# Kernel optimization log

Hardware: AMD Instinct MI355X
Metric: run time of the kernel (lower is better)

## Reference

```python
import jax, jax.numpy as jnp
import numpy as np

B, C, T = 4, 256, 4096
EPS = 1e-5
NEG = -1e8


def setup_inputs() -> dict:
    key = jax.random.key(0)
    ks = jax.random.split(key, 12)
    s = 1.0 / np.sqrt(C)
    x = jax.random.normal(ks[0], (B, C, T), dtype=jnp.float32)
    x_mask = (jax.random.uniform(ks[1], (B, 1, T)) > 0.1).astype(jnp.float32)
    return {
        "x": x,
        "x_mask": x_mask,
        # Normalize params
        "gamma": jnp.ones((C,), jnp.float32),
        "beta": jnp.zeros((C,), jnp.float32),
        "Wp": jax.random.normal(ks[2], (C, C), jnp.float32) * s,
        "bp": jnp.zeros((C,), jnp.float32),
        # 1x1 conv projections (weight [C_out, C_in])
        "Wq": jax.random.normal(ks[3], (C, C), jnp.float32) * s,
        "bq": jnp.zeros((C,), jnp.float32),
        "Wk": jax.random.normal(ks[4], (C, C), jnp.float32) * s,
        "bk": jnp.zeros((C,), jnp.float32),
        "Wv": jax.random.normal(ks[5], (C, C), jnp.float32) * s,
        "bv": jnp.zeros((C,), jnp.float32),
        "Wo": jax.random.normal(ks[6], (C, C), jnp.float32) * s,
        "bo": jnp.zeros((C,), jnp.float32),
    }


def _conv1x1(W, b, x):
    # x: [B, C, T] -> [B, C, T]
    return jnp.einsum('oc,bct->bot', W, x) + b[None, :, None]


def reference(x, x_mask, gamma, beta, Wp, bp, Wq, bq, Wk, bk, Wv, bv, Wo, bo):
    m = x_mask  # [B,1,T]
    h = x * m
    # Normalize: layer_norm over channel dim + linear, operating on [B,T,C]
    ht = h.transpose(0, 2, 1)  # [B,T,C]
    mu = jnp.mean(ht, axis=-1, keepdims=True)
    var = jnp.mean(jnp.square(ht - mu), axis=-1, keepdims=True)
    ln = (ht - mu) * jax.lax.rsqrt(var + EPS) * gamma + beta
    ln = ln @ Wp.T + bp
    h = ln.transpose(0, 2, 1) * m  # [B,C,T]

    q = _conv1x1(Wq, bq, h) * m
    k = _conv1x1(Wk, bk, h) * m
    v = _conv1x1(Wv, bv, h) * m

    scale = float(C) ** (-0.5)
    # scores[b,t,s] = sum_c q[b,c,t] k[b,c,s]
    w = jnp.einsum('bct,bcs->bts', q, k) * scale
    neg = (1.0 - m) * NEG  # [B,1,T]
    w = w + neg + neg.transpose(0, 2, 1)  # mask keys and queries
    w = jax.nn.softmax(w, axis=2)
    # h_[b,c,t] = sum_s v[b,c,s] w[b,t,s]
    h = jnp.einsum('bcs,bts->bct', v, w)
    h = _conv1x1(Wo, bo, h) * m
    return (x + h) * m
```

## Files before the change

kernel.cpp:

```cpp
#include <hip/hip_runtime.h>

#define Bn 4
#define Cn 256
#define Tn 4096

typedef unsigned short u16;
typedef __bf16 bf16x8 __attribute__((ext_vector_type(8)));
typedef float f32x4 __attribute__((ext_vector_type(4)));
typedef float f32x16 __attribute__((ext_vector_type(16)));
typedef u16 u16x8 __attribute__((ext_vector_type(8)));

__device__ __forceinline__ float b2f(u16 u) {
    union { unsigned int i; float f; } v;
    v.i = ((unsigned int)u) << 16;
    return v.f;
}
__device__ __forceinline__ u16 f2b(float f) {
    union { float f; unsigned int i; } v;
    v.f = f;
    unsigned int r = v.i + 0x7FFFu + ((v.i >> 16) & 1u);
    return (u16)(r >> 16);
}
__device__ __forceinline__ bf16x8 ones8() {
    union { u16 u[8]; bf16x8 v; } t;
    for (int j = 0; j < 8; j++) t.u[j] = 0x3F80;
    return t.v;
}

__global__ __launch_bounds__(256) void cvt_kernel(
    const float* __restrict__ w0, const float* __restrict__ w1,
    const float* __restrict__ w2, const float* __restrict__ w3,
    const float* __restrict__ w4, u16* __restrict__ dst)
{
    int gid = blockIdx.x * 256 + threadIdx.x;
    int base = gid * 4;
    int region = base >> 16;
    int off = base & 65535;
    const float* src = region == 0 ? w0 : region == 1 ? w1
                     : region == 2 ? w2 : region == 3 ? w3 : w4;
    float sc = (region == 1) ? 0.0625f : 1.0f;
    float4 v = *(const float4*)(src + off);
    ushort4 o;
    o.x = f2b(v.x * sc); o.y = f2b(v.y * sc);
    o.z = f2b(v.z * sc); o.w = f2b(v.w * sc);
    *(ushort4*)(dst + base) = o;
}

__global__ __launch_bounds__(256) void ln_kernel(
    const float* __restrict__ x, const float* __restrict__ mask,
    const float* __restrict__ gamma, const float* __restrict__ beta,
    u16* __restrict__ lnT, u16* __restrict__ xb)
{
    __shared__ __attribute__((aligned(16))) u16 tile[32][264];
    __shared__ float ssum[8][32], ssq[8][32], smu[32], srs[32];
    const int tid = threadIdx.x;
    const int b = blockIdx.y;
    const int t0 = blockIdx.x * 32;
    const int g = tid >> 5, tl = tid & 31;
    const int t = t0 + tl;
    const float mval = mask[b * Tn + t];
    float s = 0.f, s2 = 0.f;
    for (int c = g; c < Cn; c += 8) {
        float v = x[((size_t)(b * Cn + c)) * Tn + t] * mval;
        s += v; s2 += v * v;
        u16 vb = f2b(v);
        tile[tl][c] = vb;
        xb[((size_t)(b * Cn + c)) * Tn + t] = vb;
    }
    ssum[g][tl] = s; ssq[g][tl] = s2;
    __syncthreads();
    if (tid < 32) {
        float su = 0.f, sq = 0.f;
        for (int k = 0; k < 8; k++) { su += ssum[k][tid]; sq += ssq[k][tid]; }
        float mu = su * (1.f / Cn);
        float var = sq * (1.f / Cn) - mu * mu;
        var = fmaxf(var, 0.0f);
        smu[tid] = mu;
        srs[tid] = 1.0f / sqrtf(var + 1e-5f);
    }
    __syncthreads();
    for (int it = 0; it < 4; it++) {
        int idx = it * 256 + tid;
        int row = idx >> 5, c16 = idx & 31;
        float mu = smu[row], rs = srs[row];
        u16x8 ov;
        for (int j = 0; j < 8; j++) {
            int c = c16 * 8 + j;
            float h = b2f(tile[row][c]);
            float v = (h - mu) * rs * gamma[c] + beta[c];
            ov[j] = f2b(v);
        }
        *(u16x8*)(lnT + ((size_t)(b * Tn + t0 + row)) * Cn + c16 * 8) = ov;
    }
}

__global__ __launch_bounds__(256) void wp_kernel(
    const u16* __restrict__ Xb, const u16* __restrict__ Wb,
    const float* __restrict__ bias, const float* __restrict__ mask,
    u16* __restrict__ Yout)
{
    __shared__ __attribute__((aligned(16))) u16 Al[128][72];
    __shared__ __attribute__((aligned(16))) u16 Bl[64][72];
    const int tid = threadIdx.x;
    const int b = blockIdx.z;
    const int m0 = blockIdx.x * 128;
    const int n0 = blockIdx.y * 64;
    const int wave = tid >> 6, lane = tid & 63;
    const int ln16 = lane & 15, quad = lane >> 4;
    const int wm = (wave & 1) * 64, wn = (wave >> 1) * 32;

    const u16* Abase = Xb + ((size_t)(b * Tn + m0)) * Cn;
    const u16* Bbase = Wb + (size_t)n0 * Cn;

    f32x4 acc[4][2];
    for (int i = 0; i < 4; i++)
        for (int j = 0; j < 2; j++) acc[i][j] = (f32x4){0.f, 0.f, 0.f, 0.f};

    for (int k0 = 0; k0 < Cn; k0 += 64) {
        for (int it = 0; it < 4; it++) {
            int idx = it * 256 + tid;
            int row = idx >> 3, gg = idx & 7;
            *(uint4*)(&Al[row][gg * 8]) =
                *(const uint4*)(Abase + (size_t)row * Cn + k0 + gg * 8);
        }
        for (int it = 0; it < 2; it++) {
            int idx = it * 256 + tid;
            int row = idx >> 3, gg = idx & 7;
            *(uint4*)(&Bl[row][gg * 8]) =
                *(const uint4*)(Bbase + (size_t)row * Cn + k0 + gg * 8);
        }
        __syncthreads();
        for (int kk = 0; kk < 2; kk++) {
            bf16x8 af[4], bfr[2];
            for (int i = 0; i < 4; i++)
                af[i] = *(const bf16x8*)(&Al[wm + i * 16 + ln16][kk * 32 + quad * 8]);
            for (int j = 0; j < 2; j++)
                bfr[j] = *(const bf16x8*)(&Bl[wn + j * 16 + ln16][kk * 32 + quad * 8]);
            for (int i = 0; i < 4; i++)
                for (int j = 0; j < 2; j++)
                    acc[i][j] = __builtin_amdgcn_mfma_f32_16x16x32_bf16(
                        af[i], bfr[j], acc[i][j], 0, 0, 0);
        }
        __syncthreads();
    }
    for (int i = 0; i < 4; i++) {
        for (int j = 0; j < 2; j++) {
            int nn = n0 + wn + j * 16 + ln16;
            for (int r = 0; r < 4; r++) {
                int tt = m0 + wm + i * 16 + quad * 4 + r;
                float val = acc[i][j][r] + bias[nn];
                val *= mask[b * Tn + tt];
                Yout[((size_t)(b * Tn + tt)) * Cn + nn] = f2b(val);
            }
        }
    }
}

__global__ __launch_bounds__(256) void qkv_kernel(
    const u16* __restrict__ h1T,
    const u16* __restrict__ Wq_, const float* __restrict__ bq_,
    const u16* __restrict__ Wk_, const float* __restrict__ bk_,
    const u16* __restrict__ Wv_, const float* __restrict__ bv_,
    const float* __restrict__ mask,
    u16* __restrict__ qO, u16* __restrict__ kO, u16* __restrict__ vO)
{
    __shared__ __attribute__((aligned(16))) u16 Al[128][72];
    __shared__ __attribute__((aligned(16))) u16 Bl[64][72];
    const int tid = threadIdx.x;
    const int z = blockIdx.z;
    const int which = z >> 2;
    const int b = z & 3;
    const u16* W = which == 0 ? Wq_ : which == 1 ? Wk_ : Wv_;
    const float* bi = which == 0 ? bq_ : which == 1 ? bk_ : bv_;
    const float bsc = which == 0 ? 0.0625f : 1.0f;
    const int m0 = blockIdx.x * 128;
    const int n0 = blockIdx.y * 64;
    const int wave = tid >> 6, lane = tid & 63;
    const int ln16 = lane & 15, quad = lane >> 4;
    const int wm = (wave & 1) * 64, wn = (wave >> 1) * 32;

    const u16* Abase = h1T + ((size_t)(b * Tn + m0)) * Cn;
    const u16* Bbase = W + (size_t)n0 * Cn;

    f32x4 acc[4][2];
    for (int i = 0; i < 4; i++)
        for (int j = 0; j < 2; j++) acc[i][j] = (f32x4){0.f, 0.f, 0.f, 0.f};

    for (int k0 = 0; k0 < Cn; k0 += 64) {
        for (int it = 0; it < 4; it++) {
            int idx = it * 256 + tid;
            int row = idx >> 3, gg = idx & 7;
            *(uint4*)(&Al[row][gg * 8]) =
                *(const uint4*)(Abase + (size_t)row * Cn + k0 + gg * 8);
        }
        for (int it = 0; it < 2; it++) {
            int idx = it * 256 + tid;
            int row = idx >> 3, gg = idx & 7;
            *(uint4*)(&Bl[row][gg * 8]) =
                *(const uint4*)(Bbase + (size_t)row * Cn + k0 + gg * 8);
        }
        __syncthreads();
        for (int kk = 0; kk < 2; kk++) {
            bf16x8 af[4], bfr[2];
            for (int i = 0; i < 4; i++)
                af[i] = *(const bf16x8*)(&Al[wm + i * 16 + ln16][kk * 32 + quad * 8]);
            for (int j = 0; j < 2; j++)
                bfr[j] = *(const bf16x8*)(&Bl[wn + j * 16 + ln16][kk * 32 + quad * 8]);
            for (int i = 0; i < 4; i++)
                for (int j = 0; j < 2; j++)
                    acc[i][j] = __builtin_amdgcn_mfma_f32_16x16x32_bf16(
                        af[i], bfr[j], acc[i][j], 0, 0, 0);
        }
        __syncthreads();
    }

    if (which < 2) {
        u16* Yo = which == 0 ? qO : kO;
        for (int i = 0; i < 4; i++) {
            for (int j = 0; j < 2; j++) {
                int nn = n0 + wn + j * 16 + ln16;
                for (int r = 0; r < 4; r++) {
                    int tt = m0 + wm + i * 16 + quad * 4 + r;
                    float val = acc[i][j][r] + bi[nn] * bsc;
                    val *= mask[b * Tn + tt];
                    Yo[((size_t)(b * Tn + tt)) * Cn + nn] = f2b(val);
                }
            }
        }
    } else {
        u16* vt = &Al[0][0];
        for (int i = 0; i < 4; i++) {
            for (int j = 0; j < 2; j++) {
                int nl = wn + j * 16 + ln16;
                for (int r = 0; r < 4; r++) {
                    int ml = wm + i * 16 + quad * 4 + r;
                    int tt = m0 + ml;
                    float val = acc[i][j][r] + bi[n0 + nl];
                    val *= mask[b * Tn + tt];
                    vt[nl * 136 + ml] = f2b(val);
                }
            }
        }
        __syncthreads();
        for (int itc = 0; itc < 4; itc++) {
            int cidx = itc * 256 + tid;
            int row = cidx >> 4;
            int ch = cidx & 15;
            u16x8 ov = *(const u16x8*)(vt + row * 136 + ch * 8);
            *(u16x8*)(vO + ((size_t)(b * Cn + n0 + row)) * Tn + m0 + ch * 8) = ov;
        }
    }
}

__global__ __launch_bounds__(512, 2) void attn_kernel(
    const u16* __restrict__ qT, const u16* __restrict__ kT,
    const u16* __restrict__ vv, const float* __restrict__ mask,
    u16* __restrict__ PO01, u16* __restrict__ POx, float* __restrict__ pL)
{
    __shared__ __attribute__((aligned(16))) u16 kls[2][32][264];
    __shared__ __attribute__((aligned(16))) u16 vls[2][256][40];
    __shared__ __attribute__((aligned(16))) u16 pls[8][32][40];
    __shared__ float nls[1024];
    const int tid = threadIdx.x;
    const int id = blockIdx.x;
    const int spl = id & 3;
    const int b = (id >> 2) & 3;
    const int qb = id >> 4;
    const int t0 = qb * 256;
    const int wave = tid >> 6, lane = tid & 63;
    const int ln32 = lane & 31, half = lane >> 5;
    const int sBeg = spl * (Tn / 4);
    const int nIter = (Tn / 4) / 32;

    for (int i = tid; i < 1024; i += 512)
        nls[i] = (1.0f - mask[b * Tn + sBeg + i]) * -1e8f - 8.0f;

    bf16x8 qf[16];
    {
        const u16* qp = qT + ((size_t)(b * Tn + t0 + wave * 32 + ln32)) * Cn + half * 8;
        for (int ks = 0; ks < 16; ks++) qf[ks] = *(const bf16x8*)(qp + ks * 16);
    }
    f32x16 acc[8], lac;
    for (int i = 0; i < 16; i++) lac[i] = 0.f;
    for (int nt = 0; nt < 8; nt++) acc[nt] = lac;
    const bf16x8 ones = ones8();

    uint4 kpre[2], vpre[2];
    auto loadK = [&](int s0) {
        for (int i = 0; i < 2; i++) {
            int idx = i * 512 + tid;
            kpre[i] = *(const uint4*)(kT + ((size_t)(b * Tn + s0 + (idx >> 5))) * Cn + (idx & 31) * 8);
        }
    };
    auto loadV = [&](int s0) {
        for (int i = 0; i < 2; i++) {
            int idx = i * 512 + tid;
            vpre[i] = *(const uint4*)(vv + ((size_t)(b * Cn + (idx >> 2))) * Tn + s0 + (idx & 3) * 8);
        }
    };
    loadK(sBeg);
    loadV(sBeg);

    for (int it = 0; it < nIter; it++) {
        const int s0 = sBeg + it * 32;
        const int cb = it & 1;
        for (int i = 0; i < 2; i++) {
            int idx = i * 512 + tid;
            *(uint4*)(&kls[cb][idx >> 5][(idx & 31) * 8]) = kpre[i];
        }
        for (int i = 0; i < 2; i++) {
            int idx = i * 512 + tid;
            *(uint4*)(&vls[cb][idx >> 2][(idx & 3) * 8]) = vpre[i];
        }
        if (it + 1 < nIter) {
            loadK(s0 + 32);
            loadV(s0 + 32);
        }
        __syncthreads();
        const float negk = nls[it * 32 + ln32];

        f32x16 S;
        for (int i = 0; i < 16; i++) S[i] = 0.f;
        for (int ks = 0; ks < 16; ks++) {
            bf16x8 kf = *(const bf16x8*)(&kls[cb][ln32][ks * 16 + half * 8]);
            S = __builtin_amdgcn_mfma_f32_32x32x16_bf16(qf[ks], kf, S, 0, 0, 0);
        }
        for (int r = 0; r < 16; r++) S[r] = __expf(S[r] + negk);
        for (int r = 0; r < 16; r++) {
            int row = (r & 3) + 8 * (r >> 2) + 4 * half;
            pls[wave][row][ln32] = f2b(S[r]);
        }
        bf16x8 pf0 = *(const bf16x8*)(&pls[wave][ln32][half * 8]);
        bf16x8 pf1 = *(const bf16x8*)(&pls[wave][ln32][16 + half * 8]);
        lac = __builtin_amdgcn_mfma_f32_32x32x16_bf16(pf0, ones, lac, 0, 0, 0);
        lac = __builtin_amdgcn_mfma_f32_32x32x16_bf16(pf1, ones, lac, 0, 0, 0);
        for (int nt = 0; nt < 8; nt++) {
            bf16x8 v0 = *(const bf16x8*)(&vls[cb][nt * 32 + ln32][half * 8]);
            bf16x8 v1 = *(const bf16x8*)(&vls[cb][nt * 32 + ln32][16 + half * 8]);
            acc[nt] = __builtin_amdgcn_mfma_f32_32x32x16_bf16(pf0, v0, acc[nt], 0, 0, 0);
            acc[nt] = __builtin_amdgcn_mfma_f32_32x32x16_bf16(pf1, v1, acc[nt], 0, 0, 0);
        }
    }
    const size_t SZe = (size_t)Bn * Tn * Cn;
    u16* myPO = (spl < 2) ? PO01 + (size_t)spl * SZe
                          : POx + (size_t)(spl - 2) * SZe;
    for (int r = 0; r < 16; r++) {
        int trow = (r & 3) + 8 * (r >> 2) + 4 * half;
        int t = t0 + wave * 32 + trow;
        for (int nt = 0; nt < 8; nt++)
            myPO[((size_t)(b * Tn + t)) * Cn + nt * 32 + ln32] = f2b(acc[nt][r]);
        if (ln32 == 0) pL[(size_t)spl * (Bn * Tn) + b * Tn + t] = lac[r];
    }
}

__global__ __launch_bounds__(256) void final_kernel(
    const u16* __restrict__ WoB, const float* __restrict__ bo,
    const u16* __restrict__ PO01, const u16* __restrict__ POx,
    const float* __restrict__ pL,
    const float* __restrict__ mask, const u16* __restrict__ xb,
    float* __restrict__ out)
{
    __shared__ __attribute__((aligned(16))) u16 Al[128][72];
    __shared__ __attribute__((aligned(16))) u16 Bl[64][72];
    __shared__ float rls[64];
    const int tid = threadIdx.x;
    const int b = blockIdx.z;
    const int m0 = blockIdx.x * 128;
    const int n0 = blockIdx.y * 64;
    const int wave = tid >> 6, lane = tid & 63;
    const int ln16 = lane & 15, quad = lane >> 4;
    const int wm = (wave & 1) * 64, wn = (wave >> 1) * 32;
    const size_t BT = (size_t)Bn * Tn;
    const size_t SZe = BT * Cn;

    if (tid < 64) {
        size_t R = (size_t)b * Tn + n0 + tid;
        float l = pL[R] + pL[BT + R] + pL[2 * BT + R] + pL[3 * BT + R];
        rls[tid] = 1.0f / fmaxf(l, 1e-30f);
    }

    f32x4 acc[4][2];
    for (int i = 0; i < 4; i++)
        for (int j = 0; j < 2; j++) acc[i][j] = (f32x4){0.f, 0.f, 0.f, 0.f};

    for (int k0 = 0; k0 < Cn; k0 += 64) {
        for (int it = 0; it < 4; it++) {
            int idx = it * 256 + tid;
            int row = idx >> 3, gg = idx & 7;
            *(uint4*)(&Al[row][gg * 8]) =
                *(const uint4*)(WoB + (size_t)(m0 + row) * Cn + k0 + gg * 8);
        }
        for (int it = 0; it < 2; it++) {
            int idx = it * 256 + tid;
            int row = idx >> 3, gg = idx & 7;
            size_t base = ((size_t)b * Tn + n0 + row) * Cn + k0 + gg * 8;
            u16x8 a0 = *(const u16x8*)(PO01 + base);
            u16x8 a1 = *(const u16x8*)(PO01 + SZe + base);
            u16x8 a2 = *(const u16x8*)(POx + base);
            u16x8 a3 = *(const u16x8*)(POx + SZe + base);
            u16x8 o;
            for (int j = 0; j < 8; j++)
                o[j] = f2b(b2f(a0[j]) + b2f(a1[j]) + b2f(a2[j]) + b2f(a3[j]));
            *(u16x8*)(&Bl[row][gg * 8]) = o;
        }
        __syncthreads();
        for (int kk = 0; kk < 2; kk++) {
            bf16x8 af[4], bfr[2];
            for (int i = 0; i < 4; i++)
                af[i] = *(const bf16x8*)(&Al[wm + i * 16 + ln16][kk * 32 + quad * 8]);
            for (int j = 0; j < 2; j++)
                bfr[j] = *(const bf16x8*)(&Bl[wn + j * 16 + ln16][kk * 32 + quad * 8]);
            for (int i = 0; i < 4; i++)
                for (int j = 0; j < 2; j++)
                    acc[i][j] = __builtin_amdgcn_mfma_f32_16x16x32_bf16(
                        af[i], bfr[j], acc[i][j], 0, 0, 0);
        }
        __syncthreads();
    }
    for (int i = 0; i < 4; i++) {
        for (int j = 0; j < 2; j++) {
            int nl = wn + j * 16 + ln16;
            int tt = n0 + nl;
            float rl = rls[nl];
            float mk = mask[b * Tn + tt];
            for (int r = 0; r < 4; r++) {
                int oo = m0 + wm + i * 16 + quad * 4 + r;
                float val = acc[i][j][r] * rl + bo[oo];
                float xr = b2f(xb[((size_t)(b * Cn + oo)) * Tn + tt]);
                out[((size_t)(b * Cn + oo)) * Tn + tt] = (xr + val) * mk;
            }
        }
    }
}

extern "C" void kernel_launch(void* const* d_in, const int* in_sizes, int n_in,
                              void* d_out, int out_size, void* d_ws, size_t ws_size,
                              hipStream_t stream)
{
    const float* x     = (const float*)d_in[0];
    const float* xmask = (const float*)d_in[1];
    const float* gamma = (const float*)d_in[2];
    const float* beta  = (const float*)d_in[3];
    const float* Wp = (const float*)d_in[4];
    const float* bp = (const float*)d_in[5];
    const float* Wq = (const float*)d_in[6];
    const float* bq = (const float*)d_in[7];
    const float* Wk = (const float*)d_in[8];
    const float* bk = (const float*)d_in[9];
    const float* Wv = (const float*)d_in[10];
    const float* bv = (const float*)d_in[11];
    const float* Wo = (const float*)d_in[12];
    const float* bo = (const float*)d_in[13];
    float* out = (float*)d_out;

    u16* ws = (u16*)d_ws;
    const size_t SZ = (size_t)Bn * Tn * Cn;
    const size_t WSZ = (size_t)Cn * Cn;
    const size_t BT = (size_t)Bn * Tn;
    u16* lnT = ws;
    u16* h1T = ws + SZ;
    u16* qTt = ws + 2 * SZ;
    u16* kTt = ws + 3 * SZ;
    u16* vB  = ws + 4 * SZ;
    u16* wbf = ws + 5 * SZ;
    u16* PO01 = ws;
    u16* POx  = ws + 5 * SZ + 5 * WSZ;
    float* pL = (float*)(POx + 2 * SZ);
    u16* xb   = (u16*)(pL + 4 * BT);

    u16* WpB = wbf;
    u16* WqB = wbf + WSZ;
    u16* WkB = wbf + 2 * WSZ;
    u16* WvB = wbf + 3 * WSZ;
    u16* WoB = wbf + 4 * WSZ;

    dim3 blk(256);
    cvt_kernel<<<dim3(320), blk, 0, stream>>>(Wp, Wq, Wk, Wv, Wo, wbf);
    ln_kernel<<<dim3(Tn / 32, Bn), blk, 0, stream>>>(x, xmask, gamma, beta, lnT, xb);
    wp_kernel<<<dim3(Tn / 128, Cn / 64, Bn), blk, 0, stream>>>(
        lnT, WpB, bp, xmask, h1T);
    qkv_kernel<<<dim3(Tn / 128, Cn / 64, 3 * Bn), blk, 0, stream>>>(
        h1T, WqB, bq, WkB, bk, WvB, bv, xmask, qTt, kTt, vB);
    attn_kernel<<<dim3(256), dim3(512), 0, stream>>>(
        qTt, kTt, vB, xmask, PO01, POx, pL);
    final_kernel<<<dim3(Cn / 128, Tn / 64, Bn), blk, 0, stream>>>(
        WoB, bo, PO01, POx, pL, xmask, xb, out);
}
```

Measured before the change: 245.6 us.

## Register-prefetch GEMM tiles, keep attention P in registers, relax barriers

The projection, QKV and output GEMMs now load the next K-tile from global memory into registers before the barrier, so the fetch overlaps the current MFMA work. __syncthreads is replaced by a barrier that waits only on LDS counters, so outstanding global prefetches are not drained. In the attention kernel, QK^T is computed transposed so the exp'd scores can be packed to bf16 with v_cvt_pk_bf16_f32 and rearranged with v_permlane32_swap, which removes the LDS round-trip and the pls buffer. s_setprio hints raise wave priority around MFMA blocks. The cost is more register pressure, and correctness now depends on the custom barrier and on the lane mapping of the permlane swap.

Result: slower. 315.8 us (+28.6%).

```diff
diff --git a/kernel.cpp b/kernel.cpp
--- a/kernel.cpp
+++ b/kernel.cpp
@@ -25,6 +25,21 @@
     union { u16 u[8]; bf16x8 v; } t;
     for (int j = 0; j < 8; j++) t.u[j] = 0x3F80;
     return t.v;
+}
+
+__device__ __forceinline__ void barrier_nodrain() {
+    asm volatile("s_waitcnt lgkmcnt(0)" ::: "memory");
+    __builtin_amdgcn_s_barrier();
+    asm volatile("" ::: "memory");
+}
+
+__device__ __forceinline__ unsigned int cvtpk(float lo, float hi) {
+    unsigned int r;
+    asm("v_cvt_pk_bf16_f32 %0, %1, %2" : "=v"(r) : "v"(lo), "v"(hi));
+    return r;
+}
+__device__ __forceinline__ void permswap(unsigned int& a, unsigned int& b) {
+    asm("v_permlane32_swap_b32 %0, %1" : "+v"(a), "+v"(b));
 }
 
 __global__ __launch_bounds__(256) void cvt_kernel(
@@ -116,20 +131,36 @@
     for (int i = 0; i < 4; i++)
         for (int j = 0; j < 2; j++) acc[i][j] = (f32x4){0.f, 0.f, 0.f, 0.f};
 
+    uint4 pa[4], pb[2];
+    auto ldA = [&](int k0) {
+        for (int it = 0; it < 4; it++) {
+            int idx = it * 256 + tid;
+            int row = idx >> 3, gg = idx & 7;
+            pa[it] = *(const uint4*)(Abase + (size_t)row * Cn + k0 + gg * 8);
+        }
+    };
+    auto ldB = [&](int k0) {
+        for (int it = 0; it < 2; it++) {
+            int idx = it * 256 + tid;
+            int row = idx >> 3, gg = idx & 7;
+            pb[it] = *(const uint4*)(Bbase + (size_t)row * Cn + k0 + gg * 8);
+        }
+    };
+    ldA(0); ldB(0);
+
     for (int k0 = 0; k0 < Cn; k0 += 64) {
         for (int it = 0; it < 4; it++) {
             int idx = it * 256 + tid;
             int row = idx >> 3, gg = idx & 7;
-            *(uint4*)(&Al[row][gg * 8]) =
-                *(const uint4*)(Abase + (size_t)row * Cn + k0 + gg * 8);
+            *(uint4*)(&Al[row][gg * 8]) = pa[it];
         }
         for (int it = 0; it < 2; it++) {
             int idx = it * 256 + tid;
             int row = idx >> 3, gg = idx & 7;
-            *(uint4*)(&Bl[row][gg * 8]) =
-                *(const uint4*)(Bbase + (size_t)row * Cn + k0 + gg * 8);
-        }
-        __syncthreads();
+            *(uint4*)(&Bl[row][gg * 8]) = pb[it];
+        }
+        if (k0 + 64 < Cn) { ldA(k0 + 64); ldB(k0 + 64); }
+        barrier_nodrain();
         for (int kk = 0; kk < 2; kk++) {
             bf16x8 af[4], bfr[2];
             for (int i = 0; i < 4; i++)
@@ -141,7 +172,7 @@
                     acc[i][j] = __builtin_amdgcn_mfma_f32_16x16x32_bf16(
                         af[i], bfr[j], acc[i][j], 0, 0, 0);
         }
-        __syncthreads();
+        barrier_nodrain();
     }
     for (int i = 0; i < 4; i++) {
         for (int j = 0; j < 2; j++) {
@@ -186,20 +217,36 @@
     for (int i = 0; i < 4; i++)
         for (int j = 0; j < 2; j++) acc[i][j] = (f32x4){0.f, 0.f, 0.f, 0.f};
 
+    uint4 pa[4], pb[2];
+    auto ldA = [&](int k0) {
+        for (int it = 0; it < 4; it++) {
+            int idx = it * 256 + tid;
+            int row = idx >> 3, gg = idx & 7;
+            pa[it] = *(const uint4*)(Abase + (size_t)row * Cn + k0 + gg * 8);
+        }
+    };
+    auto ldB = [&](int k0) {
+        for (int it = 0; it < 2; it++) {
+            int idx = it * 256 + tid;
+            int row = idx >> 3, gg = idx & 7;
+            pb[it] = *(const uint4*)(Bbase + (size_t)row * Cn + k0 + gg * 8);
+        }
+    };
+    ldA(0); ldB(0);
+
     for (int k0 = 0; k0 < Cn; k0 += 64) {
         for (int it = 0; it < 4; it++) {
             int idx = it * 256 + tid;
             int row = idx >> 3, gg = idx & 7;
-            *(uint4*)(&Al[row][gg * 8]) =
-                *(const uint4*)(Abase + (size_t)row * Cn + k0 + gg * 8);
+            *(uint4*)(&Al[row][gg * 8]) = pa[it];
         }
         for (int it = 0; it < 2; it++) {
             int idx = it * 256 + tid;
             int row = idx >> 3, gg = idx & 7;
-            *(uint4*)(&Bl[row][gg * 8]) =
-                *(const uint4*)(Bbase + (size_t)row * Cn + k0 + gg * 8);
-        }
-        __syncthreads();
+            *(uint4*)(&Bl[row][gg * 8]) = pb[it];
+        }
+        if (k0 + 64 < Cn) { ldA(k0 + 64); ldB(k0 + 64); }
+        barrier_nodrain();
         for (int kk = 0; kk < 2; kk++) {
             bf16x8 af[4], bfr[2];
             for (int i = 0; i < 4; i++)
@@ -211,7 +258,7 @@
                     acc[i][j] = __builtin_amdgcn_mfma_f32_16x16x32_bf16(
                         af[i], bfr[j], acc[i][j], 0, 0, 0);
         }
-        __syncthreads();
+        barrier_nodrain();
     }
 
     if (which < 2) {
@@ -241,7 +288,7 @@
                 }
             }
         }
-        __syncthreads();
+        barrier_nodrain();
         for (int itc = 0; itc < 4; itc++) {
             int cidx = itc * 256 + tid;
             int row = cidx >> 4;
@@ -259,8 +306,7 @@
 {
     __shared__ __attribute__((aligned(16))) u16 kls[2][32][264];
     __shared__ __attribute__((aligned(16))) u16 vls[2][256][40];
-    __shared__ __attribute__((aligned(16))) u16 pls[8][32][40];
-    __shared__ float nls[1024];
+    __shared__ __attribute__((aligned(16))) float nls[1024];
     const int tid = threadIdx.x;
     const int id = blockIdx.x;
     const int spl = id & 3;
@@ -302,7 +348,6 @@
     loadV(sBeg);
 
     for (int it = 0; it < nIter; it++) {
-        const int s0 = sBeg + it * 32;
         const int cb = it & 1;
         for (int i = 0; i < 2; i++) {
             int idx = i * 512 + tid;
@@ -313,25 +358,44 @@
             *(uint4*)(&vls[cb][idx >> 2][(idx & 3) * 8]) = vpre[i];
         }
         if (it + 1 < nIter) {
-            loadK(s0 + 32);
-            loadV(s0 + 32);
-        }
-        __syncthreads();
-        const float negk = nls[it * 32 + ln32];
+            loadK(sBeg + (it + 1) * 32);
+            loadV(sBeg + (it + 1) * 32);
+        }
+        barrier_nodrain();
 
         f32x16 S;
         for (int i = 0; i < 16; i++) S[i] = 0.f;
+        __builtin_amdgcn_s_setprio(1);
         for (int ks = 0; ks < 16; ks++) {
             bf16x8 kf = *(const bf16x8*)(&kls[cb][ln32][ks * 16 + half * 8]);
-            S = __builtin_amdgcn_mfma_f32_32x32x16_bf16(qf[ks], kf, S, 0, 0, 0);
-        }
-        for (int r = 0; r < 16; r++) S[r] = __expf(S[r] + negk);
-        for (int r = 0; r < 16; r++) {
-            int row = (r & 3) + 8 * (r >> 2) + 4 * half;
-            pls[wave][row][ln32] = f2b(S[r]);
-        }
-        bf16x8 pf0 = *(const bf16x8*)(&pls[wave][ln32][half * 8]);
-        bf16x8 pf1 = *(const bf16x8*)(&pls[wave][ln32][16 + half * 8]);
+            S = __builtin_amdgcn_mfma_f32_32x32x16_bf16(kf, qf[ks], S, 0, 0, 0);
+        }
+        __builtin_amdgcn_s_setprio(0);
+
+        for (int g2 = 0; g2 < 4; g2++) {
+            f32x4 nk = *(const f32x4*)(&nls[it * 32 + g2 * 8 + half * 4]);
+            for (int j = 0; j < 4; j++) {
+                int r = g2 * 4 + j;
+                S[r] = __expf(S[r] + nk[j]);
+            }
+        }
+
+        union { unsigned int w[4]; bf16x8 v; } P0, P1;
+        {
+            unsigned int a0 = cvtpk(S[0], S[1]),  b0 = cvtpk(S[4], S[5]);
+            permswap(a0, b0);
+            unsigned int a1 = cvtpk(S[2], S[3]),  b1 = cvtpk(S[6], S[7]);
+            permswap(a1, b1);
+            P0.w[0] = a0; P0.w[1] = a1; P0.w[2] = b0; P0.w[3] = b1;
+            unsigned int a2 = cvtpk(S[8], S[9]),  b2 = cvtpk(S[12], S[13]);
+            permswap(a2, b2);
+            unsigned int a3 = cvtpk(S[10], S[11]), b3 = cvtpk(S[14], S[15]);
+            permswap(a3, b3);
+            P1.w[0] = a2; P1.w[1] = a3; P1.w[2] = b2; P1.w[3] = b3;
+        }
+        bf16x8 pf0 = P0.v, pf1 = P1.v;
+
+        __builtin_amdgcn_s_setprio(1);
         lac = __builtin_amdgcn_mfma_f32_32x32x16_bf16(pf0, ones, lac, 0, 0, 0);
         lac = __builtin_amdgcn_mfma_f32_32x32x16_bf16(pf1, ones, lac, 0, 0, 0);
         for (int nt = 0; nt < 8; nt++) {
@@ -340,6 +404,7 @@
             acc[nt] = __builtin_amdgcn_mfma_f32_32x32x16_bf16(pf0, v0, acc[nt], 0, 0, 0);
             acc[nt] = __builtin_amdgcn_mfma_f32_32x32x16_bf16(pf1, v1, acc[nt], 0, 0, 0);
         }
+        __builtin_amdgcn_s_setprio(0);
     }
     const size_t SZe = (size_t)Bn * Tn * Cn;
     u16* myPO = (spl < 2) ? PO01 + (size_t)spl * SZe
@@ -383,27 +448,44 @@
     for (int i = 0; i < 4; i++)
         for (int j = 0; j < 2; j++) acc[i][j] = (f32x4){0.f, 0.f, 0.f, 0.f};
 
+    uint4 pa[4];
+    u16x8 q0[2], q1[2], q2[2], q3[2];
+    auto ldA = [&](int k0) {
+        for (int it = 0; it < 4; it++) {
+            int idx = it * 256 + tid;
+            int row = idx >> 3, gg = idx & 7;
+            pa[it] = *(const uint4*)(WoB + (size_t)(m0 + row) * Cn + k0 + gg * 8);
+        }
+    };
+    auto ldB = [&](int k0) {
+        for (int it = 0; it < 2; it++) {
+            int idx = it * 256 + tid;
+            int row = idx >> 3, gg = idx & 7;
+            size_t base = ((size_t)b * Tn + n0 + row) * Cn + k0 + gg * 8;
+            q0[it] = *(const u16x8*)(PO01 + base);
+            q1[it] = *(const u16x8*)(PO01 + SZe + base);
+            q2[it] = *(const u16x8*)(POx + base);
+            q3[it] = *(const u16x8*)(POx + SZe + base);
+        }
+    };
+    ldA(0); ldB(0);
+
     for (int k0 = 0; k0 < Cn; k0 += 64) {
         for (int it = 0; it < 4; it++) {
             int idx = it * 256 + tid;
             int row = idx >> 3, gg = idx & 7;
-            *(uint4*)(&Al[row][gg * 8]) =
-                *(const uint4*)(WoB + (size_t)(m0 + row) * Cn + k0 + gg * 8);
+            *(uint4*)(&Al[row][gg * 8]) = pa[it];
         }
         for (int it = 0; it < 2; it++) {
             int idx = it * 256 + tid;
             int row = idx >> 3, gg = idx & 7;
-            size_t base = ((size_t)b * Tn + n0 + row) * Cn + k0 + gg * 8;
-            u16x8 a0 = *(const u16x8*)(PO01 + base);
-            u16x8 a1 = *(const u16x8*)(PO01 + SZe + base);
-            u16x8 a2 = *(const u16x8*)(POx + base);
-            u16x8 a3 = *(const u16x8*)(POx + SZe + base);
             u16x8 o;
             for (int j = 0; j < 8; j++)
-                o[j] = f2b(b2f(a0[j]) + b2f(a1[j]) + b2f(a2[j]) + b2f(a3[j]));
+                o[j] = f2b(b2f(q0[it][j]) + b2f(q1[it][j]) + b2f(q2[it][j]) + b2f(q3[it][j]));
             *(u16x8*)(&Bl[row][gg * 8]) = o;
         }
-        __syncthreads();
+        if (k0 + 64 < Cn) { ldA(k0 + 64); ldB(k0 + 64); }
+        barrier_nodrain();
         for (int kk = 0; kk < 2; kk++) {
             bf16x8 af[4], bfr[2];
             for (int i = 0; i < 4; i++)
@@ -415,7 +497,7 @@
                     acc[i][j] = __builtin_amdgcn_mfma_f32_16x16x32_bf16(
                         af[i], bfr[j], acc[i][j], 0, 0, 0);
         }
-        __syncthreads();
+        barrier_nodrain();
     }
     for (int i = 0; i < 4; i++) {
         for (int j = 0; j < 2; j++) {
```
